# Optimization experiments

Hardware: AMD Instinct MI355X
Metric: run time of the kernel (lower is better)

The kernel has to match this reference:

```python
import jax, jax.numpy as jnp
import numpy as np

CHEB_K = 3


def setup_inputs() -> dict:
    key = jax.random.key(0)
    k1, k2, k3 = jax.random.split(key, 3)
    B, N, C = 64, 2048, 64
    E, O = 16, 64
    x = jax.random.normal(k1, (B, N, C), dtype=jnp.float32)
    node_embeddings = jax.random.normal(k2, (N, E), dtype=jnp.float32)
    # xavier-uniform-like init for weights_pool (embed_dim, cheb_k, dim_in, dim_out)
    fan_in, fan_out = E * CHEB_K * C, O
    limit = float(np.sqrt(6.0 / (fan_in + fan_out)))
    weights_pool = jax.random.uniform(k3, (E, CHEB_K, C, O), dtype=jnp.float32,
                                      minval=-limit, maxval=limit)
    bias_pool = jnp.zeros((E, O), dtype=jnp.float32)
    return {"x": x, "node_embeddings": node_embeddings,
            "weights_pool": weights_pool, "bias_pool": bias_pool}


def reference(x, node_embeddings, weights_pool, bias_pool):
    N = node_embeddings.shape[0]
    # adaptive adjacency: softmax(relu(E E^T)) row-wise   [N, N]
    supports = jax.nn.softmax(jax.nn.relu(node_embeddings @ node_embeddings.T), axis=1)
    # Chebyshev recurrence: T0 = I, T1 = A, Tk = 2*A*T_{k-1} - T_{k-2}
    support_set = [jnp.eye(N, dtype=supports.dtype), supports]
    for _ in range(2, CHEB_K):
        support_set.append(2.0 * supports @ support_set[-1] - support_set[-2])
    supports_k = jnp.stack(support_set, axis=0)  # [K, N, N]
    # per-node dynamic weights / bias from pools
    weights = jnp.einsum('nd,dkio->nkio', node_embeddings, weights_pool)  # [N,K,C,O]
    bias = node_embeddings @ bias_pool                                    # [N,O]
    # graph conv: gather Chebyshev features then per-node grouped GEMM
    x_g = jnp.einsum('knm,bmc->bnkc', supports_k, x)       # [B,N,K,C]
    x_gconv = jnp.einsum('bnki,nkio->bno', x_g, weights) + bias  # [B,N,O]
    return x_gconv
```

## Files before the change

### kernel.cpp

```cpp
#include <hip/hip_runtime.h>
#include <hip/hip_bf16.h>

#define BB 64
#define NN 2048
#define CC 64
#define EE 16
#define OO 64
#define JJ 4096

typedef __attribute__((ext_vector_type(8))) short short8;
typedef __attribute__((ext_vector_type(4))) float f32x4;
typedef __attribute__((ext_vector_type(4))) unsigned short u16x4;
typedef __attribute__((ext_vector_type(8))) unsigned short u16x8;

__device__ __forceinline__ unsigned short f2bf(float f) {
  __hip_bfloat16 h = __float2bfloat16(f);
  return *reinterpret_cast<unsigned short*>(&h);
}
__device__ __forceinline__ float bf2f(unsigned short u) {
  unsigned int v = ((unsigned int)u) << 16;
  return *reinterpret_cast<float*>(&v);
}
__device__ __forceinline__ void gload16(const void* g, void* l) {
  __builtin_amdgcn_global_load_lds(
      (const __attribute__((address_space(1))) unsigned int*)g,
      (__attribute__((address_space(3))) unsigned int*)l, 16, 0, 0);
}

__global__ __launch_bounds__(256) void supports_kernel(
    const float* __restrict__ emb, unsigned short* __restrict__ A)
{
  int n = blockIdx.x;
  int tid = threadIdx.x;
  float en[EE];
#pragma unroll
  for (int d = 0; d < EE; ++d) en[d] = emb[n*EE + d];

  float logit[8];
  float lmax = 0.0f;
#pragma unroll
  for (int i = 0; i < 8; ++i) {
    int m = i*256 + tid;
    const float* em = emb + m*EE;
    float s = 0.f;
#pragma unroll
    for (int d = 0; d < EE; ++d) s = fmaf(en[d], em[d], s);
    s = fmaxf(s, 0.f);
    logit[i] = s;
    lmax = fmaxf(lmax, s);
  }
  __shared__ float red[256];
  red[tid] = lmax; __syncthreads();
  for (int s = 128; s > 0; s >>= 1) {
    if (tid < s) red[tid] = fmaxf(red[tid], red[tid+s]);
    __syncthreads();
  }
  lmax = red[0]; __syncthreads();
  float sum = 0.f;
#pragma unroll
  for (int i = 0; i < 8; ++i) {
    float e = __expf(logit[i]-lmax);
    logit[i] = e; sum += e;
  }
  red[tid] = sum; __syncthreads();
  for (int s = 128; s > 0; s >>= 1) {
    if (tid < s) red[tid] += red[tid+s];
    __syncthreads();
  }
  float inv = 1.f/red[0];
#pragma unroll
  for (int i = 0; i < 8; ++i) A[(size_t)n*NN + i*256 + tid] = f2bf(logit[i]*inv);
}

__global__ __launch_bounds__(256) void xpose_kernel(
    const float* __restrict__ x, unsigned short* __restrict__ Xt)
{
  int b = blockIdx.y;
  int n0 = blockIdx.x * 64;
  __shared__ float T[64][65];
  int tid = threadIdx.x;
  int r = tid >> 4, c4 = (tid & 15) * 4;
  const float* src = x + ((size_t)b*NN + n0)*64;
#pragma unroll
  for (int rr = r; rr < 64; rr += 16) {
    float4 v = *(const float4*)(src + rr*64 + c4);
    T[rr][c4] = v.x; T[rr][c4+1] = v.y; T[rr][c4+2] = v.z; T[rr][c4+3] = v.w;
  }
  __syncthreads();
  int c = tid >> 2, q0 = (tid & 3) * 16;
  unsigned short* dst = Xt + ((size_t)b*64 + c)*NN + n0 + q0;
  u16x8 o0, o1;
#pragma unroll
  for (int q = 0; q < 8; ++q) o0[q] = f2bf(T[q0+q][c]);
#pragma unroll
  for (int q = 0; q < 8; ++q) o1[q] = f2bf(T[q0+8+q][c]);
  *(u16x8*)(dst) = o0;
  *(u16x8*)(dst + 8) = o1;
}

__device__ __forceinline__ void stage_tile(
    const unsigned short* __restrict__ A, const unsigned short* __restrict__ Bt,
    unsigned short* as, unsigned short* bs,
    int m0, int j0, int k0, int wid, int lrow, int lu)
{
#pragma unroll
  for (int li = 0; li < 4; ++li) {
    int rb = wid*32 + li*8;
    int r = rb + lrow;
    int su = lu ^ (r & 7);
    gload16(A  + (size_t)(m0 + r)*2048 + k0 + su*8, as + rb*64);
    gload16(Bt + (size_t)(j0 + r)*2048 + k0 + su*8, bs + rb*64);
  }
}

__global__ __launch_bounds__(256) void gemm_bt_bf16(
    const unsigned short* __restrict__ A, const unsigned short* __restrict__ Bt,
    unsigned short* __restrict__ Crow, unsigned short* __restrict__ Ct, int writeT)
{
  __shared__ unsigned short As[2][128*64];
  __shared__ unsigned short Bs[2][128*64];
  int tid = threadIdx.x;
  int bid = blockIdx.x;
  int swz = (bid & 7) * 64 + (bid >> 3);
  int m0 = (swz >> 5) * 128, j0 = (swz & 31) * 128;
  int wid = tid >> 6, lane = tid & 63;
  int wm = wid >> 1, wn = wid & 1;
  int fr = lane & 15, kg = lane >> 4;
  int lrow = lane >> 3, lu = lane & 7;

  f32x4 acc[4][4];
#pragma unroll
  for (int i = 0; i < 4; ++i)
#pragma unroll
    for (int j = 0; j < 4; ++j) acc[i][j] = (f32x4){0.f,0.f,0.f,0.f};

  stage_tile(A, Bt, As[0], Bs[0], m0, j0, 0, wid, lrow, lu);

  int cur = 0;
#pragma unroll 2
  for (int k0 = 0; k0 < 2048; k0 += 64) {
    if (k0 + 64 < 2048) {
      stage_tile(A, Bt, As[cur^1], Bs[cur^1], m0, j0, k0 + 64, wid, lrow, lu);
      asm volatile("s_waitcnt vmcnt(8)" ::: "memory");
    } else {
      asm volatile("s_waitcnt vmcnt(0)" ::: "memory");
    }
    __builtin_amdgcn_s_barrier();
    asm volatile("" ::: "memory");

    const unsigned short* asb = As[cur];
    const unsigned short* bsb = Bs[cur];
#pragma unroll
    for (int ks = 0; ks < 2; ++ks) {
      short8 af[4], bv[4];
#pragma unroll
      for (int i = 0; i < 4; ++i) {
        int r = wm*64 + i*16 + fr;
        int u = ((ks << 2) | kg) ^ (r & 7);
        af[i] = *(const short8*)((const char*)asb + r*128 + u*16);
      }
#pragma unroll
      for (int j = 0; j < 4; ++j) {
        int r = wn*64 + j*16 + fr;
        int u = ((ks << 2) | kg) ^ (r & 7);
        bv[j] = *(const short8*)((const char*)bsb + r*128 + u*16);
      }
#pragma unroll
      for (int i = 0; i < 4; ++i)
#pragma unroll
        for (int j = 0; j < 4; ++j)
          acc[i][j] = __builtin_amdgcn_mfma_f32_16x16x32_bf16(af[i], bv[j], acc[i][j], 0, 0, 0);
    }
    asm volatile("" ::: "memory");
    __builtin_amdgcn_s_barrier();
    cur ^= 1;
  }

  int mrow4 = (lane >> 4) * 4;
#pragma unroll
  for (int i = 0; i < 4; ++i) {
    int mbase = m0 + wm*64 + i*16 + mrow4;
#pragma unroll
    for (int j = 0; j < 4; ++j) {
      int jcol = j0 + wn*64 + j*16 + fr;
      f32x4 v = acc[i][j];
      if (writeT) {
        u16x4 pk = { f2bf(v[0]), f2bf(v[1]), f2bf(v[2]), f2bf(v[3]) };
        *(u16x4*)(Ct + (size_t)jcol*2048 + mbase) = pk;
      }
      Crow[(size_t)(mbase+0)*4096 + jcol] = f2bf(v[0]);
      Crow[(size_t)(mbase+1)*4096 + jcol] = f2bf(v[1]);
      Crow[(size_t)(mbase+2)*4096 + jcol] = f2bf(v[2]);
      Crow[(size_t)(mbase+3)*4096 + jcol] = f2bf(v[3]);
    }
  }
}

__global__ __launch_bounds__(256) void wgen_kernel(
    const float* __restrict__ emb, const float* __restrict__ wp,
    unsigned short* __restrict__ wtg)
{
  __shared__ unsigned short Wlds[4][64*72];
  __shared__ float e_s[4][16];
  int tid = threadIdx.x;
  int g = blockIdx.x, r = blockIdx.y;
  int n0 = g*4;
  if (tid < 64) e_s[tid >> 4][tid & 15] = emb[n0*16 + tid];
  __syncthreads();
  int o = tid & 63, w = tid >> 6;
  float e0[16], e1[16], e2[16], e3[16];
#pragma unroll
  for (int d = 0; d < 16; ++d) {
    e0[d] = e_s[0][d]; e1[d] = e_s[1][d]; e2[d] = e_s[2][d]; e3[d] = e_s[3][d];
  }
#pragma unroll
  for (int p = 0; p < 2; ++p) {
    int u = r*8 + p*4 + w;
    float s0[8], s1[8], s2[8], s3[8];
#pragma unroll
    for (int q = 0; q < 8; ++q) { s0[q]=0.f; s1[q]=0.f; s2[q]=0.f; s3[q]=0.f; }
    const float* wpp = wp + u*512 + o;
#pragma unroll
    for (int d = 0; d < 16; ++d) {
#pragma unroll
      for (int q = 0; q < 8; ++q) {
        float wv = wpp[d*12288 + q*64];
        s0[q] = fmaf(e0[d], wv, s0[q]);
        s1[q] = fmaf(e1[d], wv, s1[q]);
        s2[q] = fmaf(e2[d], wv, s2[q]);
        s3[q] = fmaf(e3[d], wv, s3[q]);
      }
    }
    int slot = (u & 7) ^ (o & 7);
    u16x8 r0, r1, r2, r3;
#pragma unroll
    for (int q = 0; q < 8; ++q) {
      r0[q] = f2bf(s0[q]); r1[q] = f2bf(s1[q]);
      r2[q] = f2bf(s2[q]); r3[q] = f2bf(s3[q]);
    }
    *(u16x8*)&Wlds[0][o*72 + slot*8] = r0;
    *(u16x8*)&Wlds[1][o*72 + slot*8] = r1;
    *(u16x8*)&Wlds[2][o*72 + slot*8] = r2;
    *(u16x8*)&Wlds[3][o*72 + slot*8] = r3;
  }
  __syncthreads();
  int nd = tid >> 6;
  unsigned short* dst = wtg + (size_t)(n0+nd)*12288 + o*192 + r*64;
#pragma unroll
  for (int s = 0; s < 8; ++s)
    *(u16x8*)(dst + s*8) = *(const u16x8*)&Wlds[nd][o*72 + s*8];
}

#define FNPB 2
__global__ __launch_bounds__(256) void final_mfma(
    const float* __restrict__ x, const float* __restrict__ emb,
    const float* __restrict__ bp, const unsigned short* __restrict__ wtg,
    const unsigned short* __restrict__ y1, const unsigned short* __restrict__ y2,
    float* __restrict__ out)
{
  __shared__ unsigned short As[64*192];
  __shared__ unsigned short Ws[64*192];
  int tid = threadIdx.x;
  int lane = tid & 63, wid = tid >> 6;
  int b = tid & 63, quarter = tid >> 6;
  int fr = lane & 15, kg = lane >> 4;
  int o = wid*16 + fr;

  for (int inode = 0; inode < FNPB; ++inode) {
    int n = blockIdx.x * FNPB + inode;

#pragma unroll
    for (int i = 0; i < 6; ++i) {
      int base = wid*3072 + i*512;
      gload16(wtg + (size_t)n*12288 + base + lane*8, &Ws[base]);
    }

#pragma unroll
    for (int h = 0; h < 2; ++h) {
      int ul = quarter + h*4;
      const float* xp = x + ((size_t)b*NN + n)*64 + ul*8;
      float4 xv0 = *(const float4*)(xp);
      float4 xv1 = *(const float4*)(xp + 4);
      float fx[8] = {xv0.x,xv0.y,xv0.z,xv0.w,xv1.x,xv1.y,xv1.z,xv1.w};
      u16x8 v1 = *(const u16x8*)(y1 + (size_t)n*JJ + b*64 + ul*8);
      u16x8 v2 = *(const u16x8*)(y2 + (size_t)n*JJ + b*64 + ul*8);
      u16x8 xb, t2;
#pragma unroll
      for (int q = 0; q < 8; ++q) {
        xb[q] = f2bf(fx[q]);
        t2[q] = f2bf(2.f*bf2f(v2[q]) - fx[q]);
      }
      int sw = ul ^ (b & 7);
      *(u16x8*)&As[b*192 + sw*8]        = xb;
      *(u16x8*)&As[b*192 + (8|sw)*8]    = v1;
      *(u16x8*)&As[b*192 + (16|sw)*8]   = t2;
    }
    asm volatile("s_waitcnt vmcnt(0)" ::: "memory");
    __syncthreads();

    float breg = 0.f;
#pragma unroll
    for (int d = 0; d < 16; ++d) breg = fmaf(emb[n*16 + d], bp[d*64 + o], breg);
    f32x4 acc[4];
#pragma unroll
    for (int i = 0; i < 4; ++i) acc[i] = (f32x4){breg, breg, breg, breg};

#pragma unroll
    for (int ks = 0; ks < 6; ++ks) {
      int u = ks*4 + kg;
      int ro = wid*16 + fr;
      int ub = (u & ~7) | ((u & 7) ^ (ro & 7));
      short8 bv = *(const short8*)&Ws[ro*192 + ub*8];
#pragma unroll
      for (int i = 0; i < 4; ++i) {
        int ra = i*16 + fr;
        int ua = (u & ~7) | ((u & 7) ^ (ra & 7));
        short8 af = *(const short8*)&As[ra*192 + ua*8];
        acc[i] = __builtin_amdgcn_mfma_f32_16x16x32_bf16(af, bv, acc[i], 0, 0, 0);
      }
    }
    __syncthreads();

    int mrow = (lane >> 4) * 4;
#pragma unroll
    for (int i = 0; i < 4; ++i) {
#pragma unroll
      for (int r = 0; r < 4; ++r) {
        int brow = i*16 + mrow + r;
        out[((size_t)brow*NN + n)*64 + o] = acc[i][r];
      }
    }
  }
}

extern "C" void kernel_launch(void* const* d_in, const int* in_sizes, int n_in,
                              void* d_out, int out_size, void* d_ws, size_t ws_size,
                              hipStream_t stream) {
  const float* x   = (const float*)d_in[0];
  const float* emb = (const float*)d_in[1];
  const float* wp  = (const float*)d_in[2];
  const float* bp  = (const float*)d_in[3];
  float* out = (float*)d_out;

  unsigned short* Ab  = (unsigned short*)d_ws;
  unsigned short* Y1b = Ab  + (size_t)NN*NN;
  unsigned short* Y2b = Y1b + (size_t)NN*JJ;
  unsigned short* region = Y2b + (size_t)NN*JJ;
  unsigned short* Xt  = region;
  unsigned short* Y1T = region + (size_t)JJ*NN;
  unsigned short* Wtg = region;

  supports_kernel<<<NN, 256, 0, stream>>>(emb, Ab);
  xpose_kernel<<<dim3(32, 64), 256, 0, stream>>>(x, Xt);
  dim3 g(512);
  gemm_bt_bf16<<<g, 256, 0, stream>>>(Ab, Xt,  Y1b, Y1T, 1);
  gemm_bt_bf16<<<g, 256, 0, stream>>>(Ab, Y1T, Y2b, nullptr, 0);
  wgen_kernel<<<dim3(512, 3), 256, 0, stream>>>(emb, wp, Wtg);
  final_mfma<<<NN/FNPB, 256, 0, stream>>>(x, emb, bp, Wtg, Y1b, Y2b, out);
}
```

Before: 178.1 us.

## Double-buffer weight and activation prefetch in final kernel; widen wgen node tiling

```diff
diff --git a/kernel.cpp b/kernel.cpp
--- a/kernel.cpp
+++ b/kernel.cpp
@@ -200,90 +200,100 @@
     const float* __restrict__ emb, const float* __restrict__ wp,
     unsigned short* __restrict__ wtg)
 {
-  __shared__ unsigned short Wlds[4][64*72];
-  __shared__ float e_s[4][16];
+  __shared__ unsigned short Wlds[8][64*72];
+  __shared__ float e_s[8][16];
   int tid = threadIdx.x;
   int g = blockIdx.x, r = blockIdx.y;
-  int n0 = g*4;
-  if (tid < 64) e_s[tid >> 4][tid & 15] = emb[n0*16 + tid];
+  int n0 = g*8;
+  if (tid < 128) e_s[tid >> 4][tid & 15] = emb[n0*16 + tid];
   __syncthreads();
   int o = tid & 63, w = tid >> 6;
-  float e0[16], e1[16], e2[16], e3[16];
-#pragma unroll
-  for (int d = 0; d < 16; ++d) {
-    e0[d] = e_s[0][d]; e1[d] = e_s[1][d]; e2[d] = e_s[2][d]; e3[d] = e_s[3][d];
-  }
-#pragma unroll
+#pragma unroll 1
   for (int p = 0; p < 2; ++p) {
     int u = r*8 + p*4 + w;
-    float s0[8], s1[8], s2[8], s3[8];
-#pragma unroll
-    for (int q = 0; q < 8; ++q) { s0[q]=0.f; s1[q]=0.f; s2[q]=0.f; s3[q]=0.f; }
+    float acc[8][8];
+#pragma unroll
+    for (int n = 0; n < 8; ++n)
+#pragma unroll
+      for (int q = 0; q < 8; ++q) acc[n][q] = 0.f;
     const float* wpp = wp + u*512 + o;
 #pragma unroll
     for (int d = 0; d < 16; ++d) {
-#pragma unroll
-      for (int q = 0; q < 8; ++q) {
-        float wv = wpp[d*12288 + q*64];
-        s0[q] = fmaf(e0[d], wv, s0[q]);
-        s1[q] = fmaf(e1[d], wv, s1[q]);
-        s2[q] = fmaf(e2[d], wv, s2[q]);
-        s3[q] = fmaf(e3[d], wv, s3[q]);
+      float wv[8];
+#pragma unroll
+      for (int q = 0; q < 8; ++q) wv[q] = wpp[d*12288 + q*64];
+#pragma unroll
+      for (int n = 0; n < 8; ++n) {
+        float en = e_s[n][d];
+#pragma unroll
+        for (int q = 0; q < 8; ++q) acc[n][q] = fmaf(en, wv[q], acc[n][q]);
       }
     }
     int slot = (u & 7) ^ (o & 7);
-    u16x8 r0, r1, r2, r3;
-#pragma unroll
-    for (int q = 0; q < 8; ++q) {
-      r0[q] = f2bf(s0[q]); r1[q] = f2bf(s1[q]);
-      r2[q] = f2bf(s2[q]); r3[q] = f2bf(s3[q]);
-    }
-    *(u16x8*)&Wlds[0][o*72 + slot*8] = r0;
-    *(u16x8*)&Wlds[1][o*72 + slot*8] = r1;
-    *(u16x8*)&Wlds[2][o*72 + slot*8] = r2;
-    *(u16x8*)&Wlds[3][o*72 + slot*8] = r3;
+#pragma unroll
+    for (int n = 0; n < 8; ++n) {
+      u16x8 pk;
+#pragma unroll
+      for (int q = 0; q < 8; ++q) pk[q] = f2bf(acc[n][q]);
+      *(u16x8*)&Wlds[n][o*72 + slot*8] = pk;
+    }
   }
   __syncthreads();
-  int nd = tid >> 6;
-  unsigned short* dst = wtg + (size_t)(n0+nd)*12288 + o*192 + r*64;
-#pragma unroll
-  for (int s = 0; s < 8; ++s)
-    *(u16x8*)(dst + s*8) = *(const u16x8*)&Wlds[nd][o*72 + s*8];
-}
-
-#define FNPB 2
+#pragma unroll
+  for (int half = 0; half < 2; ++half) {
+    int nd = half*4 + (tid >> 6);
+    unsigned short* dst = wtg + (size_t)(n0+nd)*12288 + o*192 + r*64;
+#pragma unroll
+    for (int s = 0; s < 8; ++s)
+      *(u16x8*)(dst + s*8) = *(const u16x8*)&Wlds[nd][o*72 + s*8];
+  }
+}
+
+#define FNPB 4
 __global__ __launch_bounds__(256) void final_mfma(
     const float* __restrict__ x, const float* __restrict__ emb,
     const float* __restrict__ bp, const unsigned short* __restrict__ wtg,
     const unsigned short* __restrict__ y1, const unsigned short* __restrict__ y2,
     float* __restrict__ out)
 {
-  __shared__ unsigned short As[64*192];
-  __shared__ unsigned short Ws[64*192];
+  __shared__ unsigned short Ws[2][12288];
+  __shared__ unsigned short As[12288];
   int tid = threadIdx.x;
   int lane = tid & 63, wid = tid >> 6;
-  int b = tid & 63, quarter = tid >> 6;
+  int b = tid & 63;
   int fr = lane & 15, kg = lane >> 4;
   int o = wid*16 + fr;
-
-  for (int inode = 0; inode < FNPB; ++inode) {
-    int n = blockIdx.x * FNPB + inode;
-
-#pragma unroll
-    for (int i = 0; i < 6; ++i) {
-      int base = wid*3072 + i*512;
-      gload16(wtg + (size_t)n*12288 + base + lane*8, &Ws[base]);
-    }
+  int nb = blockIdx.x * FNPB;
+
+  float4 rx0[2][2], rx1[2][2];
+  u16x8  ry1[2][2], ry2[2][2];
+
+#pragma unroll
+  for (int h = 0; h < 2; ++h) {
+    int ul = wid + h*4;
+    const float* xp = x + ((size_t)b*NN + nb)*64 + ul*8;
+    rx0[0][h] = *(const float4*)xp;
+    rx1[0][h] = *(const float4*)(xp + 4);
+    ry1[0][h] = *(const u16x8*)(y1 + (size_t)nb*JJ + b*64 + ul*8);
+    ry2[0][h] = *(const u16x8*)(y2 + (size_t)nb*JJ + b*64 + ul*8);
+  }
+#pragma unroll
+  for (int t = 0; t < 6; ++t) {
+    int base = wid*3072 + t*512;
+    gload16(wtg + (size_t)nb*12288 + base + lane*8, &Ws[0][base]);
+  }
+
+#pragma unroll
+  for (int i = 0; i < FNPB; ++i) {
+    int n = nb + i;
+    int cs = i & 1, ns = cs ^ 1;
 
 #pragma unroll
     for (int h = 0; h < 2; ++h) {
-      int ul = quarter + h*4;
-      const float* xp = x + ((size_t)b*NN + n)*64 + ul*8;
-      float4 xv0 = *(const float4*)(xp);
-      float4 xv1 = *(const float4*)(xp + 4);
-      float fx[8] = {xv0.x,xv0.y,xv0.z,xv0.w,xv1.x,xv1.y,xv1.z,xv1.w};
-      u16x8 v1 = *(const u16x8*)(y1 + (size_t)n*JJ + b*64 + ul*8);
-      u16x8 v2 = *(const u16x8*)(y2 + (size_t)n*JJ + b*64 + ul*8);
+      int ul = wid + h*4;
+      float fx[8] = {rx0[cs][h].x, rx0[cs][h].y, rx0[cs][h].z, rx0[cs][h].w,
+                     rx1[cs][h].x, rx1[cs][h].y, rx1[cs][h].z, rx1[cs][h].w};
+      u16x8 v1 = ry1[cs][h], v2 = ry2[cs][h];
       u16x8 xb, t2;
 #pragma unroll
       for (int q = 0; q < 8; ++q) {
@@ -291,45 +301,67 @@
         t2[q] = f2bf(2.f*bf2f(v2[q]) - fx[q]);
       }
       int sw = ul ^ (b & 7);
-      *(u16x8*)&As[b*192 + sw*8]        = xb;
-      *(u16x8*)&As[b*192 + (8|sw)*8]    = v1;
-      *(u16x8*)&As[b*192 + (16|sw)*8]   = t2;
-    }
-    asm volatile("s_waitcnt vmcnt(0)" ::: "memory");
-    __syncthreads();
+      *(u16x8*)&As[b*192 + sw*8]      = xb;
+      *(u16x8*)&As[b*192 + (8|sw)*8]  = v1;
+      *(u16x8*)&As[b*192 + (16|sw)*8] = t2;
+    }
+    if (i + 1 < FNPB) {
+#pragma unroll
+      for (int h = 0; h < 2; ++h) {
+        int ul = wid + h*4;
+        const float* xp = x + ((size_t)b*NN + (n+1))*64 + ul*8;
+        rx0[ns][h] = *(const float4*)xp;
+        rx1[ns][h] = *(const float4*)(xp + 4);
+        ry1[ns][h] = *(const u16x8*)(y1 + (size_t)(n+1)*JJ + b*64 + ul*8);
+        ry2[ns][h] = *(const u16x8*)(y2 + (size_t)(n+1)*JJ + b*64 + ul*8);
+      }
+      asm volatile("s_waitcnt vmcnt(8)" ::: "memory");
+    } else {
+      asm volatile("s_waitcnt vmcnt(0)" ::: "memory");
+    }
+    asm volatile("s_waitcnt lgkmcnt(0)" ::: "memory");
+    __builtin_amdgcn_s_barrier();
+    asm volatile("" ::: "memory");
 
     float breg = 0.f;
 #pragma unroll
     for (int d = 0; d < 16; ++d) breg = fmaf(emb[n*16 + d], bp[d*64 + o], breg);
     f32x4 acc[4];
 #pragma unroll
-    for (int i = 0; i < 4; ++i) acc[i] = (f32x4){breg, breg, breg, breg};
+    for (int k = 0; k < 4; ++k) acc[k] = (f32x4){breg, breg, breg, breg};
 
 #pragma unroll
     for (int ks = 0; ks < 6; ++ks) {
       int u = ks*4 + kg;
       int ro = wid*16 + fr;
       int ub = (u & ~7) | ((u & 7) ^ (ro & 7));
-      short8 bv = *(const short8*)&Ws[ro*192 + ub*8];
-#pragma unroll
-      for (int i = 0; i < 4; ++i) {
-        int ra = i*16 + fr;
+      short8 bv = *(const short8*)&Ws[cs][ro*192 + ub*8];
+#pragma unroll
+      for (int k = 0; k < 4; ++k) {
+        int ra = k*16 + fr;
         int ua = (u & ~7) | ((u & 7) ^ (ra & 7));
         short8 af = *(const short8*)&As[ra*192 + ua*8];
-        acc[i] = __builtin_amdgcn_mfma_f32_16x16x32_bf16(af, bv, acc[i], 0, 0, 0);
-      }
-    }
-    __syncthreads();
-
+        acc[k] = __builtin_amdgcn_mfma_f32_16x16x32_bf16(af, bv, acc[k], 0, 0, 0);
+      }
+    }
     int mrow = (lane >> 4) * 4;
 #pragma unroll
-    for (int i = 0; i < 4; ++i) {
-#pragma unroll
-      for (int r = 0; r < 4; ++r) {
-        int brow = i*16 + mrow + r;
-        out[((size_t)brow*NN + n)*64 + o] = acc[i][r];
-      }
-    }
+    for (int k = 0; k < 4; ++k) {
+#pragma unroll
+      for (int rr = 0; rr < 4; ++rr) {
+        int brow = k*16 + mrow + rr;
+        out[((size_t)brow*NN + n)*64 + o] = acc[k][rr];
+      }
+    }
+    if (i + 1 < FNPB) {
+#pragma unroll
+      for (int t = 0; t < 6; ++t) {
+        int base = wid*3072 + t*512;
+        gload16(wtg + (size_t)(n+1)*12288 + base + lane*8, &Ws[ns][base]);
+      }
+    }
+    asm volatile("" ::: "memory");
+    __builtin_amdgcn_s_barrier();
   }
 }
 
@@ -355,6 +387,6 @@
   dim3 g(512);
   gemm_bt_bf16<<<g, 256, 0, stream>>>(Ab, Xt,  Y1b, Y1T, 1);
   gemm_bt_bf16<<<g, 256, 0, stream>>>(Ab, Y1T, Y2b, nullptr, 0);
-  wgen_kernel<<<dim3(512, 3), 256, 0, stream>>>(emb, wp, Wtg);
+  wgen_kernel<<<dim3(256, 3), 256, 0, stream>>>(emb, wp, Wtg);
   final_mfma<<<NN/FNPB, 256, 0, stream>>>(x, emb, bp, Wtg, Y1b, Y2b, out);
 }
```

Result: slower. 181.8 us (+2.0%).
